# Optimization experiments

Measured on AMD Instinct MI355X. Metric: run time of the kernel, lower is better.

The kernel has to match this reference:

```python
import jax, jax.numpy as jnp
import numpy as np

B, C, N, K, OUT = 4, 192, 10000, 16, 384

def setup_inputs() -> dict:
    key = jax.random.key(0)
    k1, k2, k3, k4 = jax.random.split(key, 4)
    x = jax.random.normal(k1, (B, C, N, 1), dtype=jnp.float32)
    edge_index = jax.random.randint(k2, (2, B, N, K), 0, N, dtype=jnp.int32)
    # 1x1x1 Conv3d weight [OUT, 2C, 1, 1, 1] collapsed to [OUT, 2C]
    fan_in = 2 * C
    weight = jax.random.normal(k3, (OUT, 2 * C), dtype=jnp.float32) / np.sqrt(fan_in)
    bias = jax.random.normal(k4, (OUT,), dtype=jnp.float32) * 0.01
    return {"x": x, "edge_index": edge_index, "weight": weight, "bias": bias}


def _gather_neighbors(x3, idx):
    # x3: [B, C, N], idx: [B, N, K] -> [B, C, N, K]
    return jax.vmap(lambda xb, ib: xb[:, ib])(x3, idx)


def reference(x, edge_index, weight, bias):
    b, c, n, _ = x.shape
    x3 = x[..., 0]                                   # [B, C, N]
    x_i = _gather_neighbors(x3, edge_index[1])       # centers  [B, C, N, K]
    x_j = _gather_neighbors(x3, edge_index[0])       # neighbors [B, C, N, K]
    x_j_max = jnp.max(x_j - x_i, axis=-1)            # max-relative, [B, C, N]
    # torch.cat([x.unsqueeze(2), x_j.unsqueeze(2)], 2).reshape(b, 2c, n, 1)
    # interleaves channels as (x_c, xj_c) pairs
    feat = jnp.stack([x3, x_j_max], axis=2).reshape(b, 2 * c, n)  # [B, 2C, N]
    out = jnp.einsum('oc,bcn->bon', weight, feat) + bias[None, :, None]
    out = jax.nn.relu(out)
    # Conv3d path: output shape [B, OUT, N, 1, 1]
    return out[..., None, None]
```

## Files before the change

### kernel.cpp

```cpp
#include <hip/hip_runtime.h>


#define NB   4
#define NC   192
#define NN   10000
#define NK   16
#define NOUT 384
#define K2C  384

typedef _Float16 f16x8 __attribute__((ext_vector_type(8)));
typedef _Float16 h2    __attribute__((ext_vector_type(2)));
typedef float    f32x4 __attribute__((ext_vector_type(4)));

__device__ inline unsigned short f2h(float f) {
    _Float16 h = (_Float16)f;
    return __builtin_bit_cast(unsigned short, h);
}
__device__ inline h2 hlo(unsigned int u) { return __builtin_bit_cast(h2, (unsigned int)(u & 0xFFFFu)); }

__global__ __launch_bounds__(256) void k_prep(const float* __restrict__ x,
                                              const float* __restrict__ w,
                                              unsigned short* __restrict__ xT,
                                              unsigned short* __restrict__ wh) {
    __shared__ unsigned short tile[NC * 65];
    int gid = blockIdx.x * 256 + threadIdx.x;
    if (gid < NOUT * K2C) wh[gid] = f2h(w[gid]);

    int b  = blockIdx.x & 3;
    int nb = (blockIdx.x >> 2) * 64;
    int t  = threadIdx.x;
    const float* xb = x + (size_t)b * NC * NN;
    for (int i = 0; i < 48; ++i) {
        int idx = i * 256 + t;
        int c  = idx >> 6;
        int nl = idx & 63;
        int n  = nb + nl;
        float v = (n < NN) ? xb[(size_t)c * NN + n] : 0.f;
        tile[c * 65 + nl] = f2h(v);
    }
    __syncthreads();
    unsigned int* xTd = (unsigned int*)(xT + (size_t)b * NN * NC);
    for (int i = 0; i < 24; ++i) {
        int idx = i * 256 + t;
        int nl  = idx / 96;
        int cd  = idx - nl * 96;
        int n   = nb + nl;
        if (n < NN) {
            unsigned int lo = tile[(2 * cd)     * 65 + nl];
            unsigned int hi = tile[(2 * cd + 1) * 65 + nl];
            xTd[(size_t)n * 96 + cd] = lo | (hi << 16);
        }
    }
}

__global__ __launch_bounds__(256, 4) void k_fused(const unsigned short* __restrict__ wh,
                                                  const unsigned short* __restrict__ xT,
                                                  const int* __restrict__ eidx,
                                                  const float* __restrict__ bias,
                                                  float* __restrict__ out) {
    __shared__ unsigned short lds[32 * 49 * 8];
    int bid  = blockIdx.x;
    int b    = bid & 3;
    int nt   = bid >> 2;
    int wv   = threadIdx.x >> 6;
    int lane = threadIdx.x & 63;

    const uint2* xr2 = (const uint2*)(xT + (size_t)b * NN * NC);
    const int* e0 = eidx + (size_t)b * NN * NK;
    const int* e1 = eidx + (size_t)NB * NN * NK + (size_t)b * NN * NK;
    int nbase = nt * 32 + wv * 8;

    int ej[2], ei[2];
#pragma unroll
    for (int i = 0; i < 2; ++i) {
        int idx = i * 64 + lane;
        int nn  = nbase + (idx >> 4);
        ej[i] = (nn < NN) ? __builtin_nontemporal_load(&e0[(size_t)nbase * NK + idx]) : 0;
        ei[i] = (nn < NN) ? __builtin_nontemporal_load(&e1[(size_t)nbase * NK + idx]) : 0;
    }
    int dc  = (lane < 48) ? lane : 47;
    bool wr = (lane < 48);

#pragma unroll 1
    for (int it = 0; it < 8; ++it) {
        int n = nbase + it;
        if (n < NN) {
            int nl = wv * 8 + it;
            uint2 jr[16], ir[16];
#pragma unroll
            for (int k = 0; k < 16; ++k) {
                int j = __builtin_amdgcn_readlane(ej[it >> 2], ((it & 3) * 16) + k);
                jr[k] = xr2[(size_t)j * 48 + dc];
            }
#pragma unroll
            for (int k = 0; k < 16; ++k) {
                int i_ = __builtin_amdgcn_readlane(ei[it >> 2], ((it & 3) * 16) + k);
                ir[k] = xr2[(size_t)i_ * 48 + dc];
            }
            uint2 cx = xr2[(size_t)n * 48 + dc];
            h2 m0 = __builtin_bit_cast(h2, 0xFC00FC00u);
            h2 m1 = m0;
#pragma unroll
            for (int k = 0; k < 16; ++k) {
                h2 dlo = __builtin_bit_cast(h2, jr[k].x) - __builtin_bit_cast(h2, ir[k].x);
                h2 dhi = __builtin_bit_cast(h2, jr[k].y) - __builtin_bit_cast(h2, ir[k].y);
                m0 = __builtin_elementwise_max(m0, dlo);
                m1 = __builtin_elementwise_max(m1, dhi);
            }
            unsigned int mb0 = __builtin_bit_cast(unsigned int, m0);
            unsigned int mb1 = __builtin_bit_cast(unsigned int, m1);
            uint4 g;
            g.x = (cx.x & 0xFFFFu) | (mb0 << 16);
            g.y = (cx.x >> 16)     | (mb0 & 0xFFFF0000u);
            g.z = (cx.y & 0xFFFFu) | (mb1 << 16);
            g.w = (cx.y >> 16)     | (mb1 & 0xFFFF0000u);
            if (wr) *(uint4*)&lds[(size_t)(nl * 49 + dc) * 8] = g;
        }
    }

    int r = lane & 15;
    int q = lane >> 4;
    const unsigned short* aptr = wh + (size_t)(wv * 96 + r) * K2C + q * 8;
    f32x4 acc[6][2];
#pragma unroll
    for (int mi = 0; mi < 6; ++mi)
#pragma unroll
        for (int ni = 0; ni < 2; ++ni)
            acc[mi][ni] = (f32x4){0.f, 0.f, 0.f, 0.f};

    __syncthreads();

#pragma unroll 2
    for (int t = 0; t < 12; ++t) {
        f16x8 a[6], bb[2];
#pragma unroll
        for (int mi = 0; mi < 6; ++mi)
            a[mi] = *(const f16x8*)(aptr + (size_t)mi * 16 * K2C + t * 32);
#pragma unroll
        for (int ni = 0; ni < 2; ++ni) {
            int row = ni * 16 + r;
            bb[ni] = *(const f16x8*)&lds[(size_t)(row * 49 + 4 * t + q) * 8];
        }
#pragma unroll
        for (int mi = 0; mi < 6; ++mi)
#pragma unroll
            for (int ni = 0; ni < 2; ++ni)
                acc[mi][ni] = __builtin_amdgcn_mfma_f32_16x16x32_f16(a[mi], bb[ni], acc[mi][ni], 0, 0, 0);
    }

    float* ob = out + (size_t)b * NOUT * NN;
#pragma unroll
    for (int mi = 0; mi < 6; ++mi) {
        int obase = wv * 96 + mi * 16 + q * 4;
        float4 b4 = *(const float4*)(bias + obase);
        float bv[4] = {b4.x, b4.y, b4.z, b4.w};
#pragma unroll
        for (int ni = 0; ni < 2; ++ni) {
            int n = nt * 32 + ni * 16 + r;
            if (n < NN) {
#pragma unroll
                for (int rr = 0; rr < 4; ++rr) {
                    float val = fmaxf(acc[mi][ni][rr] + bv[rr], 0.f);
                    __builtin_nontemporal_store(val, &ob[(size_t)(obase + rr) * NN + n]);
                }
            }
        }
    }
}

extern "C" void kernel_launch(void* const* d_in, const int* in_sizes, int n_in,
                              void* d_out, int out_size, void* d_ws, size_t ws_size,
                              hipStream_t stream) {
    const float* x    = (const float*)d_in[0];
    const int*   eidx = (const int*)d_in[1];
    const float* w    = (const float*)d_in[2];
    const float* bias = (const float*)d_in[3];
    float* out = (float*)d_out;

    unsigned short* xT = (unsigned short*)d_ws;
    unsigned short* wh = xT + (size_t)NB * NN * NC;

    hipLaunchKernelGGL(k_prep,  dim3(4 * 157), dim3(256), 0, stream, x, w, xT, wh);
    hipLaunchKernelGGL(k_fused, dim3(4 * 313), dim3(256), 0, stream, wh, xT, eidx, bias, out);
}
```

Before: 197.7 us.

## Split fused gather+GEMM into separate gather and GEMM kernels via workspace

The fused kernel is replaced by two kernels. A gather kernel computes the max-relative features for all nodes and writes the interleaved fp16 features to a padded global buffer. A GEMM kernel then stages 64-node tiles into LDS with direct global-to-LDS loads, using a rotated layout to avoid bank conflicts, and computes 64 columns per block instead of 32. This aims to decouple the latency-bound gather from the MFMA phase and raise occupancy for each. The cost is an extra round trip of the feature matrix through global memory and one more kernel launch.

```diff
diff --git a/kernel.cpp b/kernel.cpp
--- a/kernel.cpp
+++ b/kernel.cpp
@@ -7,6 +7,7 @@
 #define NK   16
 #define NOUT 384
 #define K2C  384
+#define NPAD 10112
 
 typedef _Float16 f16x8 __attribute__((ext_vector_type(8)));
 typedef _Float16 h2    __attribute__((ext_vector_type(2)));
@@ -16,7 +17,6 @@
     _Float16 h = (_Float16)f;
     return __builtin_bit_cast(unsigned short, h);
 }
-__device__ inline h2 hlo(unsigned int u) { return __builtin_bit_cast(h2, (unsigned int)(u & 0xFFFFu)); }
 
 __global__ __launch_bounds__(256) void k_prep(const float* __restrict__ x,
                                               const float* __restrict__ w,
@@ -53,98 +53,126 @@
     }
 }
 
-__global__ __launch_bounds__(256, 4) void k_fused(const unsigned short* __restrict__ wh,
-                                                  const unsigned short* __restrict__ xT,
-                                                  const int* __restrict__ eidx,
-                                                  const float* __restrict__ bias,
-                                                  float* __restrict__ out) {
-    __shared__ unsigned short lds[32 * 49 * 8];
+__global__ __launch_bounds__(512, 8) void k_gather(const unsigned short* __restrict__ xT,
+                                                   const int* __restrict__ eidx,
+                                                   unsigned short* __restrict__ featT) {
+    int bid  = blockIdx.x;
+    int b    = bid & 3;
+    int tile = bid >> 2;
+    int wv   = threadIdx.x >> 6;
+    int lane = threadIdx.x & 63;
+
+    const uint2* xr2 = (const uint2*)(xT + (size_t)b * NN * NC);
+    const int* e0 = eidx + (size_t)b * NN * NK;
+    const int* e1 = eidx + (size_t)NB * NN * NK + (size_t)b * NN * NK;
+    unsigned short* fb = featT + (size_t)b * NPAD * K2C;
+    int nbase = tile * 16 + wv * 2;
+
+    int ej = __builtin_nontemporal_load(&e0[(size_t)nbase * NK + (lane & 31)]);
+    int ei = __builtin_nontemporal_load(&e1[(size_t)nbase * NK + (lane & 31)]);
+
+    int dc  = (lane < 48) ? lane : 47;
+    bool wr = (lane < 48);
+
+#pragma unroll
+    for (int it = 0; it < 2; ++it) {
+        int n  = nbase + it;
+        uint2 jr[16], ir[16];
+#pragma unroll
+        for (int k = 0; k < 16; ++k) {
+            int j = __builtin_amdgcn_readlane(ej, it * 16 + k);
+            jr[k] = xr2[(size_t)j * 48 + dc];
+        }
+#pragma unroll
+        for (int k = 0; k < 16; ++k) {
+            int i_ = __builtin_amdgcn_readlane(ei, it * 16 + k);
+            ir[k] = xr2[(size_t)i_ * 48 + dc];
+        }
+        uint2 cx = xr2[(size_t)n * 48 + dc];
+        h2 m0 = __builtin_bit_cast(h2, 0xFC00FC00u);
+        h2 m1 = m0;
+#pragma unroll
+        for (int k = 0; k < 16; ++k) {
+            h2 dlo = __builtin_bit_cast(h2, jr[k].x) - __builtin_bit_cast(h2, ir[k].x);
+            h2 dhi = __builtin_bit_cast(h2, jr[k].y) - __builtin_bit_cast(h2, ir[k].y);
+            m0 = __builtin_elementwise_max(m0, dlo);
+            m1 = __builtin_elementwise_max(m1, dhi);
+        }
+        unsigned int mb0 = __builtin_bit_cast(unsigned int, m0);
+        unsigned int mb1 = __builtin_bit_cast(unsigned int, m1);
+        uint4 g;
+        g.x = (cx.x & 0xFFFFu) | (mb0 << 16);
+        g.y = (cx.x >> 16)     | (mb0 & 0xFFFF0000u);
+        g.z = (cx.y & 0xFFFFu) | (mb1 << 16);
+        g.w = (cx.y >> 16)     | (mb1 & 0xFFFF0000u);
+        if (wr) *(uint4*)(fb + (size_t)n * K2C + (size_t)dc * 8) = g;
+    }
+}
+
+__global__ __launch_bounds__(256, 3) void k_gemm(const unsigned short* __restrict__ wh,
+                                                 const unsigned short* __restrict__ featT,
+                                                 const float* __restrict__ bias,
+                                                 float* __restrict__ out) {
+    __shared__ unsigned short lds[64 * 48 * 8];
     int bid  = blockIdx.x;
     int b    = bid & 3;
     int nt   = bid >> 2;
     int wv   = threadIdx.x >> 6;
     int lane = threadIdx.x & 63;
-
-    const uint2* xr2 = (const uint2*)(xT + (size_t)b * NN * NC);
-    const int* e0 = eidx + (size_t)b * NN * NK;
-    const int* e1 = eidx + (size_t)NB * NN * NK + (size_t)b * NN * NK;
-    int nbase = nt * 32 + wv * 8;
-
-    int ej[2], ei[2];
-#pragma unroll
-    for (int i = 0; i < 2; ++i) {
-        int idx = i * 64 + lane;
-        int nn  = nbase + (idx >> 4);
-        ej[i] = (nn < NN) ? __builtin_nontemporal_load(&e0[(size_t)nbase * NK + idx]) : 0;
-        ei[i] = (nn < NN) ? __builtin_nontemporal_load(&e1[(size_t)nbase * NK + idx]) : 0;
-    }
-    int dc  = (lane < 48) ? lane : 47;
-    bool wr = (lane < 48);
-
-#pragma unroll 1
-    for (int it = 0; it < 8; ++it) {
-        int n = nbase + it;
-        if (n < NN) {
-            int nl = wv * 8 + it;
-            uint2 jr[16], ir[16];
-#pragma unroll
-            for (int k = 0; k < 16; ++k) {
-                int j = __builtin_amdgcn_readlane(ej[it >> 2], ((it & 3) * 16) + k);
-                jr[k] = xr2[(size_t)j * 48 + dc];
-            }
-#pragma unroll
-            for (int k = 0; k < 16; ++k) {
-                int i_ = __builtin_amdgcn_readlane(ei[it >> 2], ((it & 3) * 16) + k);
-                ir[k] = xr2[(size_t)i_ * 48 + dc];
-            }
-            uint2 cx = xr2[(size_t)n * 48 + dc];
-            h2 m0 = __builtin_bit_cast(h2, 0xFC00FC00u);
-            h2 m1 = m0;
-#pragma unroll
-            for (int k = 0; k < 16; ++k) {
-                h2 dlo = __builtin_bit_cast(h2, jr[k].x) - __builtin_bit_cast(h2, ir[k].x);
-                h2 dhi = __builtin_bit_cast(h2, jr[k].y) - __builtin_bit_cast(h2, ir[k].y);
-                m0 = __builtin_elementwise_max(m0, dlo);
-                m1 = __builtin_elementwise_max(m1, dhi);
-            }
-            unsigned int mb0 = __builtin_bit_cast(unsigned int, m0);
-            unsigned int mb1 = __builtin_bit_cast(unsigned int, m1);
-            uint4 g;
-            g.x = (cx.x & 0xFFFFu) | (mb0 << 16);
-            g.y = (cx.x >> 16)     | (mb0 & 0xFFFF0000u);
-            g.z = (cx.y & 0xFFFFu) | (mb1 << 16);
-            g.w = (cx.y >> 16)     | (mb1 & 0xFFFF0000u);
-            if (wr) *(uint4*)&lds[(size_t)(nl * 49 + dc) * 8] = g;
-        }
-    }
-
-    int r = lane & 15;
-    int q = lane >> 4;
+    int r    = lane & 15;
+    int q    = lane >> 4;
+
+    const unsigned short* fbase = featT + (size_t)b * NPAD * K2C + (size_t)(nt * 64) * K2C;
+#pragma unroll
+    for (int ii = 0; ii < 12; ++ii) {
+        int i = wv * 12 + ii;
+        unsigned int g = (unsigned int)(i * 64 + lane);
+        unsigned int n = g / 48u;
+        unsigned int p = g - n * 48u;
+        int j = (int)p - (int)((3u * n) % 48u);
+        if (j < 0) j += 48;
+        const unsigned short* src = fbase + (size_t)n * K2C + (size_t)j * 8;
+        __builtin_amdgcn_global_load_lds(
+            (const __attribute__((address_space(1))) unsigned int*)src,
+            (__attribute__((address_space(3))) unsigned int*)&lds[(size_t)i * 512],
+            16, 0, 0);
+    }
+
     const unsigned short* aptr = wh + (size_t)(wv * 96 + r) * K2C + q * 8;
-    f32x4 acc[6][2];
+
+    unsigned int nbs[4], u0[4];
+#pragma unroll
+    for (int ni = 0; ni < 4; ++ni) {
+        unsigned int n_ = ni * 16 + r;
+        nbs[ni] = n_ * 48u;
+        u0[ni]  = ((unsigned int)q + 3u * n_) % 48u;
+    }
+
+    f32x4 acc[6][4];
 #pragma unroll
     for (int mi = 0; mi < 6; ++mi)
 #pragma unroll
-        for (int ni = 0; ni < 2; ++ni)
+        for (int ni = 0; ni < 4; ++ni)
             acc[mi][ni] = (f32x4){0.f, 0.f, 0.f, 0.f};
 
     __syncthreads();
 
 #pragma unroll 2
     for (int t = 0; t < 12; ++t) {
-        f16x8 a[6], bb[2];
+        f16x8 a[6], bb[4];
 #pragma unroll
         for (int mi = 0; mi < 6; ++mi)
             a[mi] = *(const f16x8*)(aptr + (size_t)mi * 16 * K2C + t * 32);
 #pragma unroll
-        for (int ni = 0; ni < 2; ++ni) {
-            int row = ni * 16 + r;
-            bb[ni] = *(const f16x8*)&lds[(size_t)(row * 49 + 4 * t + q) * 8];
+        for (int ni = 0; ni < 4; ++ni) {
+            unsigned int u = u0[ni] + 4u * t;
+            if (u >= 48u) u -= 48u;
+            bb[ni] = *(const f16x8*)(lds + (size_t)(nbs[ni] + u) * 8);
         }
 #pragma unroll
         for (int mi = 0; mi < 6; ++mi)
 #pragma unroll
-            for (int ni = 0; ni < 2; ++ni)
+            for (int ni = 0; ni < 4; ++ni)
                 acc[mi][ni] = __builtin_amdgcn_mfma_f32_16x16x32_f16(a[mi], bb[ni], acc[mi][ni], 0, 0, 0);
     }
 
@@ -155,8 +183,8 @@
         float4 b4 = *(const float4*)(bias + obase);
         float bv[4] = {b4.x, b4.y, b4.z, b4.w};
 #pragma unroll
-        for (int ni = 0; ni < 2; ++ni) {
-            int n = nt * 32 + ni * 16 + r;
+        for (int ni = 0; ni < 4; ++ni) {
+            int n = nt * 64 + ni * 16 + r;
             if (n < NN) {
 #pragma unroll
                 for (int rr = 0; rr < 4; ++rr) {
@@ -177,9 +205,11 @@
     const float* bias = (const float*)d_in[3];
     float* out = (float*)d_out;
 
-    unsigned short* xT = (unsigned short*)d_ws;
-    unsigned short* wh = xT + (size_t)NB * NN * NC;
-
-    hipLaunchKernelGGL(k_prep,  dim3(4 * 157), dim3(256), 0, stream, x, w, xT, wh);
-    hipLaunchKernelGGL(k_fused, dim3(4 * 313), dim3(256), 0, stream, wh, xT, eidx, bias, out);
-}
+    unsigned short* xT    = (unsigned short*)d_ws;
+    unsigned short* featT = xT + (size_t)NB * NN * NC;
+    unsigned short* wh    = featT + (size_t)NB * NPAD * K2C;
+
+    hipLaunchKernelGGL(k_prep,   dim3(4 * 157), dim3(256), 0, stream, x, w, xT, wh);
+    hipLaunchKernelGGL(k_gather, dim3(4 * 625), dim3(512), 0, stream, xT, eidx, featT);
+    hipLaunchKernelGGL(k_gemm,   dim3(4 * 158), dim3(256), 0, stream, wh, featT, bias, out);
+}
```

Result: slower. 205.4 us (+3.9%).
